# Kernel optimization log

Measured on AMD Instinct MI355X. Metric: run time of the kernel, lower is better.

Reference implementation:

```python
import jax, jax.numpy as jnp
import numpy as np

DIM = 512
HEADS = 8
HEAD_DIM = DIM // HEADS
SCALE = DIM ** (-0.5)  # note: original uses full dim, not head_dim


def setup_inputs() -> dict:
    key = jax.random.key(0)
    ks = jax.random.split(key, 7)
    B, N = 4, 2048
    x = jax.random.normal(ks[0], (B, N, DIM), dtype=jnp.float32)
    A_phi = jax.random.normal(ks[1], (B, N, N), dtype=jnp.float32)
    # parameters (torch Linear: y = x @ W.T + b)
    w_qkv = jax.random.normal(ks[2], (3 * DIM, DIM), dtype=jnp.float32) * (DIM ** -0.5)
    b_qkv = jax.random.normal(ks[3], (3 * DIM,), dtype=jnp.float32) * 0.02
    w_out = jax.random.normal(ks[4], (DIM, DIM), dtype=jnp.float32) * (DIM ** -0.5)
    b_out = jax.random.normal(ks[5], (DIM,), dtype=jnp.float32) * 0.02
    gamma = jnp.array(1.0, dtype=jnp.float32)
    return {"x": x, "A_phi": A_phi, "w_qkv": w_qkv, "b_qkv": b_qkv,
            "w_out": w_out, "b_out": b_out, "gamma": gamma}


def reference(x, A_phi, w_qkv, b_qkv, w_out, b_out, gamma):
    B, N, D = x.shape
    qkv = x @ w_qkv.T + b_qkv  # [B,N,3D]
    q, k, v = jnp.split(qkv, 3, axis=-1)
    def to_heads(t):
        return t.reshape(B, N, HEADS, HEAD_DIM).transpose(0, 2, 1, 3)  # [B,H,N,d]
    q, k, v = to_heads(q), to_heads(k), to_heads(v)
    attn = jnp.einsum('bhqd,bhkd->bhqk', q, k) * SCALE
    attn = attn + gamma * A_phi[:, None, :, :]
    attn = jax.nn.softmax(attn, axis=-1)
    out = jnp.einsum('bhqk,bhkd->bhqd', attn, v)
    out = out.transpose(0, 2, 1, 3).reshape(B, N, D)
    return out @ w_out.T + b_out
```

## Files before the change

kernel.cpp:

```cpp
#include <hip/hip_runtime.h>

#define NSEQ 2048
#define SCALE 0.04419417382415922f
#define LOG2E 1.44269504088896f

typedef __attribute__((ext_vector_type(8))) short short8v;
typedef __attribute__((ext_vector_type(4))) float f32x4;

#define GLOAD_LDS16(g, l) __builtin_amdgcn_global_load_lds( \
    (const __attribute__((address_space(1))) void*)(g),     \
    (__attribute__((address_space(3))) void*)(l), 16, 0, 0)

__device__ __forceinline__ unsigned short f2bf(float f) {
    unsigned int u = __builtin_bit_cast(unsigned int, f);
    u += 0x7fff + ((u >> 16) & 1);
    return (unsigned short)(u >> 16);
}

__device__ __forceinline__ float exp2_fast(float x) {
    float r; asm("v_exp_f32 %0, %1" : "=v"(r) : "v"(x)); return r;
}

__device__ __forceinline__ unsigned int pack_bf16_rh(float a, float b) {
    unsigned int ua = __builtin_bit_cast(unsigned int, a) + 0x8000u;
    unsigned int ub = __builtin_bit_cast(unsigned int, b) + 0x8000u;
    return __builtin_amdgcn_perm(ub, ua, 0x07060302u);
}

__global__ __launch_bounds__(256) void cvt_bf16(const float* __restrict__ in,
                                                unsigned short* __restrict__ out, int n4) {
    int i = blockIdx.x * 256 + threadIdx.x;
    if (i < n4) {
        float4 v = ((const float4*)in)[i];
        ushort4 o;
        o.x = f2bf(v.x); o.y = f2bf(v.y); o.z = f2bf(v.z); o.w = f2bf(v.w);
        ((ushort4*)out)[i] = o;
    }
}

template<int MODE>
__global__ __launch_bounds__(256) void gemm_bf16(
    const unsigned short* __restrict__ A,
    const unsigned short* __restrict__ W,
    const float* __restrict__ bias,
    unsigned short* __restrict__ Qws,
    unsigned short* __restrict__ Kws,
    unsigned short* __restrict__ Vtws,
    float* __restrict__ Cout)
{
    __shared__ __attribute__((aligned(16))) unsigned short As[128 * 64];
    __shared__ __attribute__((aligned(16))) unsigned short Bs[128 * 64];

    int tid = threadIdx.x;
    int lane = tid & 63, w = tid >> 6;
    int wm = w >> 1, wn = w & 1;
    int g = lane >> 4, fr = lane & 15;
    int m0 = blockIdx.y * 128, n0 = blockIdx.x * 128;

    f32x4 acc[4][4] = {};

    for (int k0 = 0; k0 < 512; k0 += 64) {
        __syncthreads();
#pragma unroll
        for (int c = 0; c < 4; ++c) {
            int chunk = tid + c * 256;
            int row = chunk >> 3, c8 = chunk & 7;
            int gcol = (c8 ^ (row & 7)) * 8;
            GLOAD_LDS16(A + (size_t)(m0 + row) * 512 + k0 + gcol, &As[chunk * 8]);
            GLOAD_LDS16(W + (size_t)(n0 + row) * 512 + k0 + gcol, &Bs[chunk * 8]);
        }
        __syncthreads();
#pragma unroll
        for (int kk = 0; kk < 2; ++kk) {
            short8v af[4], bf[4];
#pragma unroll
            for (int mi = 0; mi < 4; ++mi) {
                int row = wm * 64 + mi * 16 + fr;
                af[mi] = *(const short8v*)(&As[row * 64 + (((kk * 4 + g) ^ (row & 7)) * 8)]);
            }
#pragma unroll
            for (int ni = 0; ni < 4; ++ni) {
                int row = wn * 64 + ni * 16 + fr;
                bf[ni] = *(const short8v*)(&Bs[row * 64 + (((kk * 4 + g) ^ (row & 7)) * 8)]);
            }
#pragma unroll
            for (int mi = 0; mi < 4; ++mi)
#pragma unroll
                for (int ni = 0; ni < 4; ++ni)
                    acc[mi][ni] = __builtin_amdgcn_mfma_f32_16x16x32_bf16(
                        af[mi], bf[ni], acc[mi][ni], 0, 0, 0);
        }
    }

#pragma unroll
    for (int mi = 0; mi < 4; ++mi) {
#pragma unroll
        for (int ni = 0; ni < 4; ++ni) {
            int col = n0 + wn * 64 + ni * 16 + fr;
            float bb = bias[col];
#pragma unroll
            for (int r = 0; r < 4; ++r) {
                int row = m0 + wm * 64 + mi * 16 + g * 4 + r;
                float val = acc[mi][ni][r] + bb;
                if (MODE == 0) {
                    int b = row >> 11, s = row & 2047;
                    if (col < 512) {
                        int h = col >> 6, d = col & 63;
                        Qws[(((size_t)(b * 8 + h) * NSEQ + s) << 6) + d] = f2bf(val * (SCALE * LOG2E));
                    } else if (col < 1024) {
                        int c2 = col - 512; int h = c2 >> 6, d = c2 & 63;
                        Kws[(((size_t)(b * 8 + h) * NSEQ + s) << 6) + d] = f2bf(val);
                    } else {
                        int c2 = col - 1024; int h = c2 >> 6, d = c2 & 63;
                        Vtws[((size_t)(b * 8 + h) * 64 + d) * NSEQ + s] = f2bf(val);
                    }
                } else {
                    Cout[(size_t)row * 512 + col] = val;
                }
            }
        }
    }
}

__global__ __launch_bounds__(512, 3) void attn_kernel(
    const unsigned short* __restrict__ Qws,
    const unsigned short* __restrict__ Kws,
    const unsigned short* __restrict__ Vtws,
    const float* __restrict__ A_phi,
    const float* __restrict__ gamma_p,
    unsigned short* __restrict__ Oout)
{
    __shared__ __attribute__((aligned(16))) unsigned short Ks[2][64 * 64];
    __shared__ __attribute__((aligned(16))) unsigned short Vts[2][64 * 64];
    __shared__ __attribute__((aligned(16))) unsigned short Pl[8][16 * 64];

    int tid = threadIdx.x, lane = tid & 63, w = tid >> 6;
    int g = lane >> 4, fr = lane & 15;

    int id = blockIdx.x;
    int b = (id & 7) >> 1, p = id & 1;
    int j = id >> 3;
    int h = j & 7;
    int qt = ((j >> 3) << 1) | p;
    int bh = b * 8 + h;
    int q0 = qt * 128 + w * 16;
    float g2 = gamma_p[0] * LOG2E;

    const unsigned short* Kb = Kws + (size_t)bh * NSEQ * 64;
    const unsigned short* Vb = Vtws + (size_t)bh * 64 * NSEQ;
    const float* Ap = A_phi + (size_t)b * NSEQ * NSEQ;

    short8v qf[2];
#pragma unroll
    for (int dc = 0; dc < 2; ++dc)
        qf[dc] = *(const short8v*)(Qws + ((size_t)bh * NSEQ + q0 + fr) * 64 + dc * 32 + g * 8);

    int c = tid;
    int krow = c >> 3;
    int kchunk = c & 7;
    int swK = (kchunk ^ ((krow >> 2) & 7)) * 8;
    int swV = (kchunk ^ (krow & 7)) * 8;
    int kcol = kchunk * 8;

    float l_lane[4] = {};
    f32x4 o_acc[4] = {};

    {
        short8v k0v = *(const short8v*)(Kb + c * 8);
        short8v v0v = *(const short8v*)(Vb + (size_t)krow * NSEQ + kcol);
        *(short8v*)(&Ks[0][krow * 64 + swK]) = k0v;
        *(short8v*)(&Vts[0][krow * 64 + swV]) = v0v;
    }
    __syncthreads();

    for (int kt = 0; kt < NSEQ / 64; ++kt) {
        int cur = kt & 1;

        short8v kreg, vreg;
        if (kt < NSEQ / 64 - 1) {
            kreg = *(const short8v*)(Kb + (kt + 1) * 4096 + c * 8);
            vreg = *(const short8v*)(Vb + (size_t)krow * NSEQ + (kt + 1) * 64 + kcol);
        }

        float4 av[4];
#pragma unroll
        for (int r = 0; r < 4; ++r)
            av[r] = *(const float4*)(Ap + (size_t)(q0 + g * 4 + r) * NSEQ + kt * 64 + 4 * fr);

        f32x4 sa[4] = {};
        __builtin_amdgcn_s_setprio(1);
#pragma unroll
        for (int kf = 0; kf < 4; ++kf) {
            int row = 4 * fr + kf;
#pragma unroll
            for (int dc = 0; dc < 2; ++dc) {
                short8v kfrag = *(const short8v*)(
                    &Ks[cur][row * 64 + (((dc * 4 + g) ^ ((row >> 2) & 7)) * 8)]);
                sa[kf] = __builtin_amdgcn_mfma_f32_16x16x32_bf16(qf[dc], kfrag, sa[kf], 0, 0, 0);
            }
        }
        __builtin_amdgcn_s_setprio(0);

#pragma unroll
        for (int r = 0; r < 4; ++r) {
            float e0 = exp2_fast(fmaf(g2, av[r].x, sa[0][r]));
            float e1 = exp2_fast(fmaf(g2, av[r].y, sa[1][r]));
            float e2 = exp2_fast(fmaf(g2, av[r].z, sa[2][r]));
            float e3 = exp2_fast(fmaf(g2, av[r].w, sa[3][r]));
            l_lane[r] += (e0 + e1) + (e2 + e3);
            int rp = g * 4 + r;
            uint2 pp;
            pp.x = pack_bf16_rh(e0, e1);
            pp.y = pack_bf16_rh(e2, e3);
            *(uint2*)(&Pl[w][rp * 64 + (((fr >> 1) ^ (rp & 7)) * 8) + (fr & 1) * 4]) = pp;
        }
        asm volatile("s_waitcnt lgkmcnt(0)" ::: "memory");

#pragma unroll
        for (int kc = 0; kc < 2; ++kc) {
            short8v pf = *(const short8v*)(
                &Pl[w][fr * 64 + (((kc * 4 + g) ^ (fr & 7)) * 8)]);
            __builtin_amdgcn_s_setprio(1);
#pragma unroll
            for (int nf = 0; nf < 4; ++nf) {
                int vrow = nf * 16 + fr;
                short8v vf = *(const short8v*)(
                    &Vts[cur][vrow * 64 + (((kc * 4 + g) ^ (vrow & 7)) * 8)]);
                o_acc[nf] = __builtin_amdgcn_mfma_f32_16x16x32_bf16(pf, vf, o_acc[nf], 0, 0, 0);
            }
            __builtin_amdgcn_s_setprio(0);
        }

        if (kt < NSEQ / 64 - 1) {
            *(short8v*)(&Ks[cur ^ 1][krow * 64 + swK]) = kreg;
            *(short8v*)(&Vts[cur ^ 1][krow * 64 + swV]) = vreg;
        }
        __syncthreads();
    }

#pragma unroll
    for (int r = 0; r < 4; ++r) {
        float l = l_lane[r];
        l += __shfl_xor(l, 1);
        l += __shfl_xor(l, 2);
        l += __shfl_xor(l, 4);
        l += __shfl_xor(l, 8);
        float inv = 1.0f / l;
        int qg = q0 + g * 4 + r;
#pragma unroll
        for (int nf = 0; nf < 4; ++nf)
            Oout[((size_t)b * NSEQ + qg) * 512 + h * 64 + nf * 16 + fr] =
                f2bf(o_acc[nf][r] * inv);
    }
}

extern "C" void kernel_launch(void* const* d_in, const int* in_sizes, int n_in,
                              void* d_out, int out_size, void* d_ws, size_t ws_size,
                              hipStream_t stream) {
    const float* x      = (const float*)d_in[0];
    const float* A_phi  = (const float*)d_in[1];
    const float* w_qkv  = (const float*)d_in[2];
    const float* b_qkv  = (const float*)d_in[3];
    const float* w_out  = (const float*)d_in[4];
    const float* b_out  = (const float*)d_in[5];
    const float* gamma  = (const float*)d_in[6];
    float* out = (float*)d_out;

    unsigned short* xb   = (unsigned short*)d_ws;
    unsigned short* wqb  = xb  + (size_t)8192 * 512;
    unsigned short* wob  = wqb + (size_t)1536 * 512;
    unsigned short* Qws  = wob + (size_t)512 * 512;
    unsigned short* Kws  = Qws + (size_t)4 * 8 * NSEQ * 64;
    unsigned short* Vtws = Kws + (size_t)4 * 8 * NSEQ * 64;
    unsigned short* Oat  = Vtws + (size_t)4 * 8 * NSEQ * 64;

    cvt_bf16<<<dim3(4096), dim3(256), 0, stream>>>(x, xb, 8192 * 512 / 4);
    cvt_bf16<<<dim3(768),  dim3(256), 0, stream>>>(w_qkv, wqb, 1536 * 512 / 4);
    cvt_bf16<<<dim3(256),  dim3(256), 0, stream>>>(w_out, wob, 512 * 512 / 4);

    gemm_bf16<0><<<dim3(12, 64), dim3(256), 0, stream>>>(
        xb, wqb, b_qkv, Qws, Kws, Vtws, nullptr);

    attn_kernel<<<dim3(512), dim3(512), 0, stream>>>(
        Qws, Kws, Vtws, A_phi, gamma, Oat);

    gemm_bf16<1><<<dim3(4, 64), dim3(256), 0, stream>>>(
        Oat, wob, b_out, nullptr, nullptr, nullptr, out);
}
```

Baseline: 124.3 us.

## Merge conversion launches, vectorize V-transpose stores, shrink output GEMM tile

Folds the three fp32-to-bf16 conversion kernels into a single launch, which removes two kernel launches. Templates the GEMM on tile size so the output projection uses 64x128 tiles and 512 blocks instead of 256, giving better CU occupancy. The transposed V stores are packed into 8-byte vector writes of four consecutive sequence elements instead of scattered 2-byte stores. Total work is unchanged, and the main cost, the attention kernel, is untouched.

```diff
diff --git a/kernel.cpp b/kernel.cpp
--- a/kernel.cpp
+++ b/kernel.cpp
@@ -27,18 +27,26 @@
     return __builtin_amdgcn_perm(ub, ua, 0x07060302u);
 }
 
-__global__ __launch_bounds__(256) void cvt_bf16(const float* __restrict__ in,
-                                                unsigned short* __restrict__ out, int n4) {
-    int i = blockIdx.x * 256 + threadIdx.x;
-    if (i < n4) {
-        float4 v = ((const float4*)in)[i];
-        ushort4 o;
-        o.x = f2bf(v.x); o.y = f2bf(v.y); o.z = f2bf(v.z); o.w = f2bf(v.w);
-        ((ushort4*)out)[i] = o;
-    }
-}
-
-template<int MODE>
+__global__ __launch_bounds__(256) void cvt_all(
+    const float* __restrict__ x, const float* __restrict__ wq,
+    const float* __restrict__ wo,
+    unsigned short* __restrict__ xb, unsigned short* __restrict__ wqb,
+    unsigned short* __restrict__ wob)
+{
+    int bid = blockIdx.x;
+    const float* in;
+    unsigned short* out;
+    int i;
+    if (bid < 4096)      { in = x;  out = xb;  i = bid * 256 + threadIdx.x; }
+    else if (bid < 4864) { in = wq; out = wqb; i = (bid - 4096) * 256 + threadIdx.x; }
+    else                 { in = wo; out = wob; i = (bid - 4864) * 256 + threadIdx.x; }
+    float4 v = ((const float4*)in)[i];
+    ushort4 o;
+    o.x = f2bf(v.x); o.y = f2bf(v.y); o.z = f2bf(v.z); o.w = f2bf(v.w);
+    ((ushort4*)out)[i] = o;
+}
+
+template<int MODE, int BM, int BN>
 __global__ __launch_bounds__(256) void gemm_bf16(
     const unsigned short* __restrict__ A,
     const unsigned short* __restrict__ W,
@@ -48,43 +56,50 @@
     unsigned short* __restrict__ Vtws,
     float* __restrict__ Cout)
 {
-    __shared__ __attribute__((aligned(16))) unsigned short As[128 * 64];
-    __shared__ __attribute__((aligned(16))) unsigned short Bs[128 * 64];
+    const int WM = BM / 2, WN = BN / 2;
+    __shared__ __attribute__((aligned(16))) unsigned short As[BM * 64];
+    __shared__ __attribute__((aligned(16))) unsigned short Bs[BN * 64];
 
     int tid = threadIdx.x;
     int lane = tid & 63, w = tid >> 6;
     int wm = w >> 1, wn = w & 1;
     int g = lane >> 4, fr = lane & 15;
-    int m0 = blockIdx.y * 128, n0 = blockIdx.x * 128;
-
-    f32x4 acc[4][4] = {};
+    int m0 = blockIdx.y * BM, n0 = blockIdx.x * BN;
+
+    f32x4 acc[WM / 16][4] = {};
 
     for (int k0 = 0; k0 < 512; k0 += 64) {
         __syncthreads();
 #pragma unroll
-        for (int c = 0; c < 4; ++c) {
+        for (int c = 0; c < BM * 8 / 256; ++c) {
             int chunk = tid + c * 256;
             int row = chunk >> 3, c8 = chunk & 7;
             int gcol = (c8 ^ (row & 7)) * 8;
             GLOAD_LDS16(A + (size_t)(m0 + row) * 512 + k0 + gcol, &As[chunk * 8]);
+        }
+#pragma unroll
+        for (int c = 0; c < BN * 8 / 256; ++c) {
+            int chunk = tid + c * 256;
+            int row = chunk >> 3, c8 = chunk & 7;
+            int gcol = (c8 ^ (row & 7)) * 8;
             GLOAD_LDS16(W + (size_t)(n0 + row) * 512 + k0 + gcol, &Bs[chunk * 8]);
         }
         __syncthreads();
 #pragma unroll
         for (int kk = 0; kk < 2; ++kk) {
-            short8v af[4], bf[4];
-#pragma unroll
-            for (int mi = 0; mi < 4; ++mi) {
-                int row = wm * 64 + mi * 16 + fr;
+            short8v af[WM / 16], bf[4];
+#pragma unroll
+            for (int mi = 0; mi < WM / 16; ++mi) {
+                int row = wm * WM + mi * 16 + fr;
                 af[mi] = *(const short8v*)(&As[row * 64 + (((kk * 4 + g) ^ (row & 7)) * 8)]);
             }
 #pragma unroll
             for (int ni = 0; ni < 4; ++ni) {
-                int row = wn * 64 + ni * 16 + fr;
+                int row = wn * WN + ni * 16 + fr;
                 bf[ni] = *(const short8v*)(&Bs[row * 64 + (((kk * 4 + g) ^ (row & 7)) * 8)]);
             }
 #pragma unroll
-            for (int mi = 0; mi < 4; ++mi)
+            for (int mi = 0; mi < WM / 16; ++mi)
 #pragma unroll
                 for (int ni = 0; ni < 4; ++ni)
                     acc[mi][ni] = __builtin_amdgcn_mfma_f32_16x16x32_bf16(
@@ -93,30 +108,37 @@
     }
 
 #pragma unroll
-    for (int mi = 0; mi < 4; ++mi) {
+    for (int mi = 0; mi < WM / 16; ++mi) {
 #pragma unroll
         for (int ni = 0; ni < 4; ++ni) {
-            int col = n0 + wn * 64 + ni * 16 + fr;
+            int col = n0 + wn * WN + ni * 16 + fr;
             float bb = bias[col];
-#pragma unroll
-            for (int r = 0; r < 4; ++r) {
-                int row = m0 + wm * 64 + mi * 16 + g * 4 + r;
-                float val = acc[mi][ni][r] + bb;
-                if (MODE == 0) {
-                    int b = row >> 11, s = row & 2047;
-                    if (col < 512) {
-                        int h = col >> 6, d = col & 63;
-                        Qws[(((size_t)(b * 8 + h) * NSEQ + s) << 6) + d] = f2bf(val * (SCALE * LOG2E));
-                    } else if (col < 1024) {
-                        int c2 = col - 512; int h = c2 >> 6, d = c2 & 63;
-                        Kws[(((size_t)(b * 8 + h) * NSEQ + s) << 6) + d] = f2bf(val);
-                    } else {
-                        int c2 = col - 1024; int h = c2 >> 6, d = c2 & 63;
-                        Vtws[((size_t)(b * 8 + h) * 64 + d) * NSEQ + s] = f2bf(val);
-                    }
+            int row0 = m0 + wm * WM + mi * 16 + g * 4;
+            if (MODE == 0) {
+                int b = row0 >> 11, s0 = row0 & 2047;
+                if (col < 512) {
+                    int h = col >> 6, d = col & 63;
+#pragma unroll
+                    for (int r = 0; r < 4; ++r)
+                        Qws[(((size_t)(b * 8 + h) * NSEQ + s0 + r) << 6) + d] =
+                            f2bf((acc[mi][ni][r] + bb) * (SCALE * LOG2E));
+                } else if (col < 1024) {
+                    int c2 = col - 512; int h = c2 >> 6, d = c2 & 63;
+#pragma unroll
+                    for (int r = 0; r < 4; ++r)
+                        Kws[(((size_t)(b * 8 + h) * NSEQ + s0 + r) << 6) + d] =
+                            f2bf(acc[mi][ni][r] + bb);
                 } else {
-                    Cout[(size_t)row * 512 + col] = val;
+                    int c2 = col - 1024; int h = c2 >> 6, d = c2 & 63;
+                    uint2 pv;
+                    pv.x = pack_bf16_rh(acc[mi][ni][0] + bb, acc[mi][ni][1] + bb);
+                    pv.y = pack_bf16_rh(acc[mi][ni][2] + bb, acc[mi][ni][3] + bb);
+                    *(uint2*)(&Vtws[((size_t)(b * 8 + h) * 64 + d) * NSEQ + s0]) = pv;
                 }
+            } else {
+#pragma unroll
+                for (int r = 0; r < 4; ++r)
+                    Cout[(size_t)(row0 + r) * 512 + col] = acc[mi][ni][r] + bb;
             }
         }
     }
@@ -274,16 +296,14 @@
     unsigned short* Vtws = Kws + (size_t)4 * 8 * NSEQ * 64;
     unsigned short* Oat  = Vtws + (size_t)4 * 8 * NSEQ * 64;
 
-    cvt_bf16<<<dim3(4096), dim3(256), 0, stream>>>(x, xb, 8192 * 512 / 4);
-    cvt_bf16<<<dim3(768),  dim3(256), 0, stream>>>(w_qkv, wqb, 1536 * 512 / 4);
-    cvt_bf16<<<dim3(256),  dim3(256), 0, stream>>>(w_out, wob, 512 * 512 / 4);
-
-    gemm_bf16<0><<<dim3(12, 64), dim3(256), 0, stream>>>(
+    cvt_all<<<dim3(5120), dim3(256), 0, stream>>>(x, w_qkv, w_out, xb, wqb, wob);
+
+    gemm_bf16<0, 128, 128><<<dim3(12, 64), dim3(256), 0, stream>>>(
         xb, wqb, b_qkv, Qws, Kws, Vtws, nullptr);
 
     attn_kernel<<<dim3(512), dim3(512), 0, stream>>>(
         Qws, Kws, Vtws, A_phi, gamma, Oat);
 
-    gemm_bf16<1><<<dim3(4, 64), dim3(256), 0, stream>>>(
+    gemm_bf16<1, 64, 128><<<dim3(4, 128), dim3(256), 0, stream>>>(
         Oat, wob, b_out, nullptr, nullptr, nullptr, out);
 }
```

Result: faster. 107.5 us (-13.5%).
